# Kernel tuning notes

Measured on AMD Instinct MI355X. Metric: run time of the kernel, lower is better.

The kernel has to match this reference:

```python
import jax, jax.numpy as jnp
import numpy as np

B, NSM, NLG = 64, 400, 196
SM, LG = 512, 1024
D, H, DH = 4, 16, 64
INNER = H * DH
EPS = 1e-5


def setup_inputs() -> dict:
    key = jax.random.key(0)
    ks = iter(jax.random.split(key, 40))
    def rn(shape, s=0.02):
        return jax.random.normal(next(ks), shape, jnp.float32) * s
    inp = {
        "sm_tokens": rn((B, NSM + 1, SM), 1.0),
        "lg_tokens": rn((B, NLG + 1, LG), 1.0),
    }
    def branch(p, din, dout):
        inp[p + "_pin_w"] = rn((D, din, dout))
        inp[p + "_pin_b"] = jnp.zeros((D, dout), jnp.float32)
        inp[p + "_ng"] = jnp.ones((D, dout), jnp.float32)
        inp[p + "_nb"] = jnp.zeros((D, dout), jnp.float32)
        inp[p + "_wq"] = rn((D, dout, INNER))
        inp[p + "_wkv"] = rn((D, dout, 2 * INNER))
        inp[p + "_wo"] = rn((D, INNER, dout))
        inp[p + "_wob"] = jnp.zeros((D, dout), jnp.float32)
        inp[p + "_pout_w"] = rn((D, dout, din))
        inp[p + "_pout_b"] = jnp.zeros((D, din), jnp.float32)
    branch("a", SM, LG)   # sm_attend_lg: project sm->lg, attention in lg_dim
    branch("b", LG, SM)   # lg_attend_sm: project lg->sm, attention in sm_dim
    return inp


def _attn(cls_tok, ctx, ng, nb, wq, wkv, wo, wob):
    # cls_tok: [B,1,dim]; ctx: [B,S,dim]. Matches lucidrains cross_vit Attention:
    # LayerNorm(x) first; kv context = concat(normed_x, context); context NOT normed.
    scale = DH ** -0.5
    mu = cls_tok.mean(-1, keepdims=True)
    var = ((cls_tok - mu) ** 2).mean(-1, keepdims=True)
    xn = (cls_tok - mu) * jax.lax.rsqrt(var + EPS) * ng + nb
    c = jnp.concatenate([xn, ctx], axis=1)             # kv_include_self=True
    q = (xn @ wq).reshape(B, 1, H, DH)
    k, v = jnp.split(c @ wkv, 2, axis=-1)
    k = k.reshape(B, -1, H, DH)
    v = v.reshape(B, -1, H, DH)
    s = jnp.einsum('bqhd,bkhd->bhqk', q, k) * scale     # [B,H,1,S+1]
    p = jax.nn.softmax(s, axis=-1)
    o = jnp.einsum('bhqk,bkhd->bqhd', p, v).reshape(B, 1, INNER)
    return o @ wo + wob


def _forward(sm_tokens, lg_tokens,
             a_pin_w, a_pin_b, a_ng, a_nb, a_wq, a_wkv, a_wo, a_wob, a_pout_w, a_pout_b,
             b_pin_w, b_pin_b, b_ng, b_nb, b_wq, b_wkv, b_wo, b_wob, b_pout_w, b_pout_b):
    sm_cls, sm_patch = sm_tokens[:, :1], sm_tokens[:, 1:]
    lg_cls, lg_patch = lg_tokens[:, :1], lg_tokens[:, 1:]
    for i in range(D):
        x = sm_cls @ a_pin_w[i] + a_pin_b[i]
        x = _attn(x, lg_patch, a_ng[i], a_nb[i], a_wq[i], a_wkv[i], a_wo[i], a_wob[i])
        sm_cls = x @ a_pout_w[i] + a_pout_b[i] + sm_cls
        y = lg_cls @ b_pin_w[i] + b_pin_b[i]
        y = _attn(y, sm_patch, b_ng[i], b_nb[i], b_wq[i], b_wkv[i], b_wo[i], b_wob[i])
        lg_cls = y @ b_pout_w[i] + b_pout_b[i] + lg_cls
    sm_out = jnp.concatenate([sm_cls, sm_patch], axis=1)
    lg_out = jnp.concatenate([lg_cls, lg_patch], axis=1)
    return sm_out, lg_out


def reference(sm_tokens, lg_tokens,
              a_pin_w, a_pin_b, a_ng, a_nb, a_wq, a_wkv, a_wo, a_wob, a_pout_w, a_pout_b,
              b_pin_w, b_pin_b, b_ng, b_nb, b_wq, b_wkv, b_wo, b_wob, b_pout_w, b_pout_b):
    return _forward(sm_tokens, lg_tokens,
                    a_pin_w, a_pin_b, a_ng, a_nb, a_wq, a_wkv, a_wo, a_wob, a_pout_w, a_pout_b,
                    b_pin_w, b_pin_b, b_ng, b_nb, b_wq, b_wkv, b_wo, b_wob, b_pout_w, b_pout_b)
```

## Files before the change

kernel.cpp:

```cpp
#include <hip/hip_runtime.h>
#include <hip/hip_bf16.h>
#include <math.h>

#define B_     64
#define NSM_   400
#define NLG_   196
#define SM_    512
#define LG_    1024
#define H_     16
#define DH_    64
#define INNER_ 1024
#define SSTR   424
#define PSTR   424
#define NJMAX  7

typedef __attribute__((ext_vector_type(8))) short bf16x8;
typedef __attribute__((ext_vector_type(8))) unsigned short u16x8;
typedef __attribute__((ext_vector_type(4))) float f32x4;

__device__ __forceinline__ unsigned short f2b(float f) {
  unsigned u = __float_as_uint(f);
  u = u + 0x7FFFu + ((u >> 16) & 1u);
  return (unsigned short)(u >> 16);
}
__device__ __forceinline__ f32x4 zero4() {
  f32x4 a; a[0] = 0.f; a[1] = 0.f; a[2] = 0.f; a[3] = 0.f; return a;
}
__device__ __forceinline__ bf16x8 ntl8(const unsigned short* p) {
  return __builtin_nontemporal_load((const bf16x8*)p);
}


struct CC2 { const float* tok; float* out; unsigned short* abf; float* cls;
             unsigned short* clsb; int Np1, nf4, shift, tot4; };
struct WTDesc { const float* src; unsigned short* dst; unsigned short* dst2; int K, N; };
struct WTArgs { WTDesc d[10]; int cum[11]; };
__global__ __launch_bounds__(256) void setup1(CC2 ca, CC2 cb, WTArgs W, int nw) {
  __shared__ unsigned short tile[64][68];
  const int tid = threadIdx.x;
  if ((int)blockIdx.x < nw) {
    int bx = blockIdx.x, di = 0;
    while (bx >= W.cum[di + 1]) di++;
    int local = bx - W.cum[di];
    WTDesc g = W.d[di];
    int tn = g.N >> 6;
    int tpl = tn * (g.K >> 6);
    int layer = local / tpl, rem = local % tpl;
    int kt = (rem / tn) * 64, nt = (rem % tn) * 64;
    const float* wp = g.src + (size_t)layer * g.K * g.N;
    unsigned short* op = g.dst + (size_t)layer * g.K * g.N;
    unsigned short* d2 = (g.dst2 && nt < 1024)
                             ? g.dst2 + (size_t)layer * g.K * 1024 : nullptr;
#pragma unroll
    for (int p = 0; p < 4; p++) {
      int r = (tid >> 4) + p * 16;
      int c = (tid & 15) * 4;
      const f32x4 v = __builtin_nontemporal_load(
          (const f32x4*)&wp[(size_t)(kt + r) * g.N + nt + c]);
      ushort4 w4;
      w4.x = f2b(v.x); w4.y = f2b(v.y); w4.z = f2b(v.z); w4.w = f2b(v.w);
      *(ushort4*)&tile[r][c] = w4;
      if (d2) *(ushort4*)&d2[(size_t)(kt + r) * 1024 + nt + c] = w4;
    }
    __syncthreads();
    const int r2 = tid >> 2, cseg = tid & 3;
    u16x8 v0, v1;
#pragma unroll
    for (int i = 0; i < 8; i++) v0[i] = tile[cseg * 16 + i][r2];
#pragma unroll
    for (int i = 0; i < 8; i++) v1[i] = tile[cseg * 16 + 8 + i][r2];
    unsigned short* orow = &op[(size_t)(nt + r2) * g.K + kt + cseg * 16];
    *(u16x8*)&orow[0] = v0;
    *(u16x8*)&orow[8] = v1;
  } else {
    const int nblk = gridDim.x - nw;
    const int total = ca.tot4 + cb.tot4;
    for (int i = ((int)blockIdx.x - nw) * 256 + tid; i < total; i += nblk * 256) {
      CC2 g; int idx;
      if (i < ca.tot4) { g = ca; idx = i; } else { g = cb; idx = i - ca.tot4; }
      int rowg = idx >> g.shift, t = idx & ((1 << g.shift) - 1);
      int bb = rowg / g.Np1, row = rowg - bb * g.Np1;
      const f32x4 v = __builtin_nontemporal_load(&((const f32x4*)g.tok)[idx]);
      __builtin_nontemporal_store(v, &((f32x4*)g.out)[idx]);
      ushort4 w2; w2.x = f2b(v.x); w2.y = f2b(v.y); w2.z = f2b(v.z); w2.w = f2b(v.w);
      if (row > 0) {
        ((ushort4*)g.abf)[(size_t)(bb * (g.Np1 - 1) + row - 1) * g.nf4 + t] = w2;
      } else {
        ((f32x4*)g.cls)[(size_t)bb * g.nf4 + t] = v;
        ((ushort4*)g.clsb)[(size_t)bb * g.nf4 + t] = w2;
      }
    }
  }
}

struct TXArgs { const unsigned short* xbf; unsigned short* xT; int Nctx, dout, xstride, nx, ny, nblk; };
__global__ __launch_bounds__(256) void setup2(TXArgs ta, TXArgs tb) {
  __shared__ unsigned short tile[64][68];
  TXArgs g; int bx = blockIdx.x;
  if (bx < ta.nblk) { g = ta; } else { g = tb; bx -= ta.nblk; }
  int cx = bx % g.nx; int rem = bx / g.nx;
  int jy = rem % g.ny; int b = rem / g.ny;
  int jt = jy * 64, ct = cx * 64;
  const int tid = threadIdx.x;
#pragma unroll
  for (int p = 0; p < 4; p++) {
    int row = (tid >> 4) + p * 16;
    int c = (tid & 15) * 4;
    int j = jt + row;
    ushort4 v;
    if (j < g.Nctx) v = *(const ushort4*)&g.xbf[((size_t)b * g.Nctx + j) * g.dout + ct + c];
    else { v.x = 0; v.y = 0; v.z = 0; v.w = 0; }
    *(ushort4*)&tile[row][c] = v;
  }
  __syncthreads();
  const int r2 = tid >> 2, jseg = tid & 3;
  if (jt + jseg * 16 < g.xstride) {
    u16x8 v0, v1;
#pragma unroll
    for (int i = 0; i < 8; i++) v0[i] = tile[jseg * 16 + i][r2];
#pragma unroll
    for (int i = 0; i < 8; i++) v1[i] = tile[jseg * 16 + 8 + i][r2];
    unsigned short* orow = &g.xT[((size_t)b * g.dout + ct + r2) * g.xstride + jt + jseg * 16];
    *(u16x8*)&orow[0] = v0;
    *(u16x8*)&orow[8] = v1;
  }
}

struct SGDesc {
  const unsigned short* A; const unsigned short* WT; const float* bias;
  float* Cf; unsigned short* Cbf; const float* Rf;
  int K, N;
  float* outF; int ostride;
};
struct SGArgs { SGDesc d[4]; int cum[5]; int nd; };
__global__ __launch_bounds__(256) void sg_wide(SGArgs W) {
  int bx = blockIdx.x, di = 0;
  while (di < W.nd - 1 && bx >= W.cum[di + 1]) di++;
  SGDesc g = W.d[di];
  const int n0 = (bx - W.cum[di]) * 16;
  const int tid = threadIdx.x;
  const int lane = tid & 63, mt = tid >> 6;
  const int r16 = lane & 15, kv8 = (lane >> 4) * 8;
  f32x4 acc0 = zero4(), acc1 = zero4();
  const unsigned short* wp = &g.WT[(size_t)(n0 + r16) * g.K + kv8];
  const unsigned short* ap = &g.A[(size_t)(mt * 16 + r16) * g.K + kv8];
  const int K = g.K;
#pragma unroll 2
  for (int k0 = 0; k0 < K; k0 += 64) {
    acc0 = __builtin_amdgcn_mfma_f32_16x16x32_bf16(*(const bf16x8*)&ap[k0],
                                                   ntl8(&wp[k0]), acc0, 0, 0, 0);
    acc1 = __builtin_amdgcn_mfma_f32_16x16x32_bf16(*(const bf16x8*)&ap[k0 + 32],
                                                   ntl8(&wp[k0 + 32]), acc1, 0, 0, 0);
  }
  const int rbase = (lane >> 4) * 4;
#pragma unroll
  for (int rr = 0; rr < 4; rr++) {
    int r = mt * 16 + rbase + rr, c = n0 + r16;
    float v = acc0[rr] + acc1[rr];
    if (g.bias) v += g.bias[c];
    if (g.Rf) v += g.Rf[(size_t)r * g.N + c];
    if (g.Cf)  g.Cf[(size_t)r * g.N + c] = v;
    if (g.Cbf) g.Cbf[(size_t)r * g.N + c] = f2b(v);
    if (g.outF) g.outF[(size_t)r * g.ostride + c] = v;
  }
}

struct LNArgs { const float* x; unsigned short* xnb; const float* ng; const float* nb; int dim; };
__global__ __launch_bounds__(256) void ln2(LNArgs la, LNArgs lb) {
  LNArgs g = ((int)blockIdx.x < 64) ? la : lb;
  int b = blockIdx.x & 63, t = threadIdx.x;
  __shared__ float rs[4], rq[4], bc[2];
  const float* xp = g.x + (size_t)b * g.dim;
  float s = 0.f, sq = 0.f;
  for (int c = t; c < g.dim; c += 256) {
    float v = xp[c];
    s += v; sq += v * v;
  }
#pragma unroll
  for (int off = 32; off >= 1; off >>= 1) {
    s += __shfl_down(s, off);
    sq += __shfl_down(sq, off);
  }
  int w = t >> 6;
  if ((t & 63) == 0) { rs[w] = s; rq[w] = sq; }
  __syncthreads();
  if (t == 0) {
    float ts = rs[0] + rs[1] + rs[2] + rs[3];
    float tq = rq[0] + rq[1] + rq[2] + rq[3];
    float mu = ts / g.dim;
    float var = tq / g.dim - mu * mu;
    bc[0] = mu; bc[1] = rsqrtf(var + 1e-5f);
  }
  __syncthreads();
  float mu = bc[0], r = bc[1];
  for (int c = t; c < g.dim; c += 256)
    g.xnb[(size_t)b * g.dim + c] = f2b((xp[c] - mu) * r * g.ng[c] + g.nb[c]);
}

struct QTArgs { const unsigned short* qb16; const unsigned short* wkvnb;
                unsigned short* qt; int dout, ntiles, nblk; };
__global__ __launch_bounds__(256) void qtilde3(QTArgs ga, QTArgs gb) {
  QTArgs g; int bx = blockIdx.x;
  if (bx < ga.nblk) g = ga; else { g = gb; bx -= ga.nblk; }
  const int h = bx / g.ntiles, nt = bx - h * g.ntiles;
  const int n0 = nt * 16;
  const int tid = threadIdx.x, lane = tid & 63, mt = tid >> 6;
  const int r16 = lane & 15, kv8 = (lane >> 4) * 8;
  const unsigned short* ap = g.qb16 + (size_t)(mt * 16 + r16) * INNER_ + h * 64 + kv8;
  const unsigned short* bp = g.wkvnb + (size_t)(n0 + r16) * 1024 + h * 64 + kv8;
  f32x4 acc0 = zero4(), acc1 = zero4();
  acc0 = __builtin_amdgcn_mfma_f32_16x16x32_bf16(*(const bf16x8*)&ap[0],
                                                 *(const bf16x8*)&bp[0], acc0, 0, 0, 0);
  acc1 = __builtin_amdgcn_mfma_f32_16x16x32_bf16(*(const bf16x8*)&ap[32],
                                                 *(const bf16x8*)&bp[32], acc1, 0, 0, 0);
  const int rbase = (lane >> 4) * 4;
#pragma unroll
  for (int rr = 0; rr < 4; rr++) {
    int b = mt * 16 + rbase + rr;
    g.qt[((size_t)b * 16 + h) * g.dout + n0 + r16] = f2b(acc0[rr] + acc1[rr]);
  }
}

struct SArgs { const unsigned short* qt; const unsigned short* xbf; float* S;
               int dout, Nctx, ntj, nbj, nblk; };
__global__ __launch_bounds__(256) void s_gemm(SArgs ga, SArgs gb) {
  SArgs g; int bx;
  if ((int)blockIdx.x < ga.nblk) { g = ga; bx = blockIdx.x; }
  else { g = gb; bx = blockIdx.x - ga.nblk; }
  const int b = bx / g.nbj, jq = bx - b * g.nbj;
  const int tid = threadIdx.x, lane = tid & 63, w = tid >> 6;
  const int jt = jq * 4 + w;
  if (jt >= g.ntj) return;
  const int r16 = lane & 15, kv8 = (lane >> 4) * 8;
  const unsigned short* ap = g.qt + ((size_t)b * 16 + r16) * g.dout + kv8;
  const unsigned short* bp = g.xbf + ((size_t)b * g.Nctx + jt * 16 + r16) * g.dout + kv8;
  f32x4 acc0 = zero4(), acc1 = zero4();
  const int K = g.dout;
#pragma unroll 2
  for (int k0 = 0; k0 < K; k0 += 64) {
    acc0 = __builtin_amdgcn_mfma_f32_16x16x32_bf16(*(const bf16x8*)&ap[k0],
                                                   *(const bf16x8*)&bp[k0], acc0, 0, 0, 0);
    acc1 = __builtin_amdgcn_mfma_f32_16x16x32_bf16(*(const bf16x8*)&ap[k0 + 32],
                                                   *(const bf16x8*)&bp[k0 + 32], acc1, 0, 0, 0);
  }
  const int rbase = (lane >> 4) * 4;
#pragma unroll
  for (int rr = 0; rr < 4; rr++)
    g.S[((size_t)b * 16 + rbase + rr) * SSTR + jt * 16 + r16] = acc0[rr] + acc1[rr];
}

struct UArgs {
  const float* S; const float* qb; const float* kvc; const unsigned short* xT;
  unsigned short* u; float* pcls; int dout, Nctx, Npad, xstride, ntc, nblk;
};
__global__ __launch_bounds__(256) void usoftmax(UArgs ga, UArgs gb) {
  __shared__ unsigned short p_s[16 * PSTR];
  UArgs g; int bx;
  if ((int)blockIdx.x < ga.nblk) { g = ga; bx = blockIdx.x; }
  else { g = gb; bx = blockIdx.x - ga.nblk; }
  const int b = bx / g.ntc, ct = bx - b * g.ntc;
  const int t = threadIdx.x, lane = t & 63, w = t >> 6;
  for (int hh = 0; hh < 4; hh++) {
    const int h = w * 4 + hh;
    const float* Sp = g.S + ((size_t)b * 16 + h) * SSTR;
    float sc = g.qb[(size_t)b * 1024 + h * 64 + lane] * g.kvc[(size_t)b * 2048 + h * 64 + lane];
#pragma unroll
    for (int o = 32; o >= 1; o >>= 1) sc += __shfl_down(sc, o);
    sc = __shfl(sc, 0) * 0.125f;
    float sv[NJMAX];
    float mr = -1e30f;
#pragma unroll
    for (int ji = 0; ji < NJMAX; ji++) {
      int j = ji * 64 + lane;
      sv[ji] = (j < g.Nctx) ? Sp[j] * 0.125f : -1e30f;
      mr = fmaxf(mr, sv[ji]);
    }
#pragma unroll
    for (int o = 32; o >= 1; o >>= 1) mr = fmaxf(mr, __shfl_down(mr, o));
    mr = __shfl(mr, 0);
    const float m = fmaxf(mr, sc);
    float es = 0.f;
#pragma unroll
    for (int ji = 0; ji < NJMAX; ji++) {
      int j = ji * 64 + lane;
      float e = (j < g.Nctx) ? expf(sv[ji] - m) : 0.f;
      sv[ji] = e; es += e;
    }
#pragma unroll
    for (int o = 32; o >= 1; o >>= 1) es += __shfl_down(es, o);
    es = __shfl(es, 0);
    const float ecls = expf(sc - m);
    const float inv = 1.f / (es + ecls);
#pragma unroll
    for (int ji = 0; ji < NJMAX; ji++) {
      int j = ji * 64 + lane;
      if (j < g.Npad) p_s[h * PSTR + j] = (j < g.Nctx) ? f2b(sv[ji] * inv) : (unsigned short)0;
    }
    if (ct == 0 && lane == 0) g.pcls[b * 16 + h] = ecls * inv;
  }
  __syncthreads();
  const int r16 = lane & 15, kv8 = (lane >> 4) * 8, rbase = (lane >> 4) * 4;
  const int c0 = ct * 64 + w * 16;
  f32x4 acc0 = zero4(), acc1 = zero4();
  const unsigned short* bp = g.xT + ((size_t)b * g.dout + c0 + r16) * g.xstride + kv8;
  const unsigned short* apl = &p_s[r16 * PSTR + kv8];
  const int Kp = g.Npad;
  int k0 = 0;
  for (; k0 + 64 <= Kp; k0 += 64) {
    acc0 = __builtin_amdgcn_mfma_f32_16x16x32_bf16(*(const bf16x8*)&apl[k0],
                                                   *(const bf16x8*)&bp[k0], acc0, 0, 0, 0);
    acc1 = __builtin_amdgcn_mfma_f32_16x16x32_bf16(*(const bf16x8*)&apl[k0 + 32],
                                                   *(const bf16x8*)&bp[k0 + 32], acc1, 0, 0, 0);
  }
  if (k0 < Kp)
    acc0 = __builtin_amdgcn_mfma_f32_16x16x32_bf16(*(const bf16x8*)&apl[k0],
                                                   *(const bf16x8*)&bp[k0], acc0, 0, 0, 0);
#pragma unroll
  for (int rr = 0; rr < 4; rr++)
    g.u[((size_t)b * 16 + rbase + rr) * g.dout + c0 + r16] = f2b(acc0[rr] + acc1[rr]);
}

struct OArgs {
  const unsigned short* u; const unsigned short* WTkv; const float* kvc; const float* pcls;
  unsigned short* ob; int dout;
};
__global__ __launch_bounds__(256) void ogemm_w(OArgs ga, OArgs gb) {
  OArgs g; int bx = blockIdx.x;
  if (bx < 64) { g = ga; } else { g = gb; bx -= 64; }
  const int h = bx >> 2, dt = bx & 3;
  const int tid = threadIdx.x, lane = tid & 63, mt = tid >> 6;
  const int r16 = lane & 15, kv8 = (lane >> 4) * 8;
  const int dout = g.dout;
  f32x4 acc0 = zero4(), acc1 = zero4();
  const unsigned short* wp = &g.WTkv[(size_t)(1024 + h * 64 + dt * 16 + r16) * dout + kv8];
  const unsigned short* up = &g.u[((size_t)(mt * 16 + r16) * 16 + h) * dout + kv8];
#pragma unroll 2
  for (int k0 = 0; k0 < dout; k0 += 64) {
    acc0 = __builtin_amdgcn_mfma_f32_16x16x32_bf16(*(const bf16x8*)&up[k0],
                                                   ntl8(&wp[k0]), acc0, 0, 0, 0);
    acc1 = __builtin_amdgcn_mfma_f32_16x16x32_bf16(*(const bf16x8*)&up[k0 + 32],
                                                   ntl8(&wp[k0 + 32]), acc1, 0, 0, 0);
  }
  const int rbase = (lane >> 4) * 4;
#pragma unroll
  for (int rr = 0; rr < 4; rr++) {
    int bi = mt * 16 + rbase + rr;
    int d = h * 64 + dt * 16 + r16;
    float v = acc0[rr] + acc1[rr] + g.pcls[bi * 16 + h] * g.kvc[(size_t)bi * 2048 + 1024 + d];
    g.ob[(size_t)bi * INNER_ + d] = f2b(v);
  }
}

extern "C" void kernel_launch(void* const* d_in, const int* in_sizes, int n_in,
                              void* d_out, int out_size, void* d_ws, size_t ws_size,
                              hipStream_t stream) {
  const float* sm_tokens = (const float*)d_in[0];
  const float* lg_tokens = (const float*)d_in[1];
  const float* a_pin_w  = (const float*)d_in[2];  const float* a_pin_b  = (const float*)d_in[3];
  const float* a_ng     = (const float*)d_in[4];  const float* a_nb     = (const float*)d_in[5];
  const float* a_wq     = (const float*)d_in[6];  const float* a_wkv    = (const float*)d_in[7];
  const float* a_wo     = (const float*)d_in[8];  const float* a_wob    = (const float*)d_in[9];
  const float* a_pout_w = (const float*)d_in[10]; const float* a_pout_b = (const float*)d_in[11];
  const float* b_pin_w  = (const float*)d_in[12]; const float* b_pin_b  = (const float*)d_in[13];
  const float* b_ng     = (const float*)d_in[14]; const float* b_nb     = (const float*)d_in[15];
  const float* b_wq     = (const float*)d_in[16]; const float* b_wkv    = (const float*)d_in[17];
  const float* b_wo     = (const float*)d_in[18]; const float* b_wob    = (const float*)d_in[19];
  const float* b_pout_w = (const float*)d_in[20]; const float* b_pout_b = (const float*)d_in[21];

  float* out = (float*)d_out;
  char* ws = (char*)d_ws;
  size_t off = 0;
  auto alloc = [&](size_t bytes) -> void* {
    void* pt = ws + off;
    off += (bytes + 255) & ~(size_t)255;
    return pt;
  };
  unsigned short* Abf_lg = (unsigned short*)alloc(((size_t)B_ * NLG_ + 32) * LG_ * 2);
  unsigned short* Abf_sm = (unsigned short*)alloc(((size_t)B_ * NSM_ + 32) * SM_ * 2);
  unsigned short* xT_lg  = (unsigned short*)alloc((size_t)B_ * LG_ * 224 * 2);
  unsigned short* xT_sm  = (unsigned short*)alloc((size_t)B_ * SM_ * 416 * 2);
  unsigned short* WTkv_a = (unsigned short*)alloc((size_t)4 * 2048 * LG_ * 2);
  unsigned short* WTkv_b = (unsigned short*)alloc((size_t)4 * 2048 * SM_ * 2);
  unsigned short* wkvnb_a = (unsigned short*)alloc((size_t)4 * LG_ * 1024 * 2);
  unsigned short* wkvnb_b = (unsigned short*)alloc((size_t)4 * SM_ * 1024 * 2);
  unsigned short* WTpin_a = (unsigned short*)alloc((size_t)4 * SM_ * LG_ * 2);
  unsigned short* WTpin_b = (unsigned short*)alloc((size_t)4 * LG_ * SM_ * 2);
  unsigned short* WTwq_a  = (unsigned short*)alloc((size_t)4 * LG_ * INNER_ * 2);
  unsigned short* WTwq_b  = (unsigned short*)alloc((size_t)4 * SM_ * INNER_ * 2);
  unsigned short* WTwo_a  = (unsigned short*)alloc((size_t)4 * INNER_ * LG_ * 2);
  unsigned short* WTwo_b  = (unsigned short*)alloc((size_t)4 * INNER_ * SM_ * 2);
  unsigned short* WTpout_a = (unsigned short*)alloc((size_t)4 * LG_ * SM_ * 2);
  unsigned short* WTpout_b = (unsigned short*)alloc((size_t)4 * SM_ * LG_ * 2);
  unsigned short* qt_a = (unsigned short*)alloc((size_t)B_ * 16 * LG_ * 2);
  unsigned short* qt_b = (unsigned short*)alloc((size_t)B_ * 16 * SM_ * 2);
  float* S_a = (float*)alloc((size_t)B_ * 16 * SSTR * 4);
  float* S_b = (float*)alloc((size_t)B_ * 16 * SSTR * 4);
  unsigned short* u_a  = (unsigned short*)alloc((size_t)B_ * 16 * LG_ * 2);
  unsigned short* u_b  = (unsigned short*)alloc((size_t)B_ * 16 * SM_ * 2);
  float* pcls_a = (float*)alloc((size_t)B_ * 16 * 4);
  float* pcls_b = (float*)alloc((size_t)B_ * 16 * 4);
  float* cls_sm = (float*)alloc((size_t)B_ * SM_ * 4);
  float* cls_lg = (float*)alloc((size_t)B_ * LG_ * 4);
  unsigned short* clsb_sm = (unsigned short*)alloc((size_t)B_ * SM_ * 2);
  unsigned short* clsb_lg = (unsigned short*)alloc((size_t)B_ * LG_ * 2);
  float* xbuf_a = (float*)alloc((size_t)B_ * LG_ * 4);
  float* xbuf_b = (float*)alloc((size_t)B_ * SM_ * 4);
  unsigned short* xnb_a = (unsigned short*)alloc((size_t)B_ * LG_ * 2);
  unsigned short* xnb_b = (unsigned short*)alloc((size_t)B_ * SM_ * 2);
  float* qbuf_a = (float*)alloc((size_t)B_ * INNER_ * 4);
  float* qbuf_b = (float*)alloc((size_t)B_ * INNER_ * 4);
  unsigned short* qb16_a = (unsigned short*)alloc((size_t)B_ * INNER_ * 2);
  unsigned short* qb16_b = (unsigned short*)alloc((size_t)B_ * INNER_ * 2);
  float* kvc_a  = (float*)alloc((size_t)B_ * 2048 * 4);
  float* kvc_b  = (float*)alloc((size_t)B_ * 2048 * 4);
  unsigned short* obufb_a = (unsigned short*)alloc((size_t)B_ * INNER_ * 2);
  unsigned short* obufb_b = (unsigned short*)alloc((size_t)B_ * INNER_ * 2);
  unsigned short* t1b_a = (unsigned short*)alloc((size_t)B_ * LG_ * 2);
  unsigned short* t1b_b = (unsigned short*)alloc((size_t)B_ * SM_ * 2);
  (void)ws_size; (void)in_sizes; (void)n_in; (void)out_size;

  const size_t sm_elems = (size_t)B_ * (NSM_ + 1) * SM_;

  CC2 ca{sm_tokens, out, Abf_sm, cls_sm, clsb_sm, NSM_ + 1, SM_ / 4, 7,
         (int)(sm_elems / 4)};
  CC2 cb{lg_tokens, out + sm_elems, Abf_lg, cls_lg, clsb_lg, NLG_ + 1, LG_ / 4, 8,
         (int)((size_t)B_ * (NLG_ + 1) * LG_ / 4)};
  WTArgs W;
  W.d[0] = {a_wkv,    WTkv_a,   wkvnb_a, LG_, 2048};
  W.d[1] = {b_wkv,    WTkv_b,   wkvnb_b, SM_, 2048};
  W.d[2] = {a_pin_w,  WTpin_a,  nullptr, SM_, LG_};
  W.d[3] = {b_pin_w,  WTpin_b,  nullptr, LG_, SM_};
  W.d[4] = {a_wq,     WTwq_a,   nullptr, LG_, INNER_};
  W.d[5] = {b_wq,     WTwq_b,   nullptr, SM_, INNER_};
  W.d[6] = {a_wo,     WTwo_a,   nullptr, INNER_, LG_};
  W.d[7] = {b_wo,     WTwo_b,   nullptr, INNER_, SM_};
  W.d[8] = {a_pout_w, WTpout_a, nullptr, LG_, SM_};
  W.d[9] = {b_pout_w, WTpout_b, nullptr, SM_, LG_};
  W.cum[0] = 0;
  for (int i = 0; i < 10; i++)
    W.cum[i + 1] = W.cum[i] + (W.d[i].K / 64) * (W.d[i].N / 64) * 4;
  setup1<<<W.cum[10] + 2048, 256, 0, stream>>>(ca, cb, W, W.cum[10]);
  TXArgs txa{Abf_lg, xT_lg, NLG_, LG_, 224, LG_ / 64, 4, B_ * (LG_ / 64) * 4};
  TXArgs txb{Abf_sm, xT_sm, NSM_, SM_, 416, SM_ / 64, 7, B_ * (SM_ / 64) * 7};
  setup2<<<txa.nblk + txb.nblk, 256, 0, stream>>>(txa, txb);

  for (int l = 0; l < 4; l++) {
    const unsigned short* WTpin_al = WTpin_a + (size_t)l * SM_ * LG_;
    const unsigned short* WTpin_bl = WTpin_b + (size_t)l * LG_ * SM_;
    const unsigned short* WTwq_al  = WTwq_a  + (size_t)l * LG_ * INNER_;
    const unsigned short* WTwq_bl  = WTwq_b  + (size_t)l * SM_ * INNER_;
    const unsigned short* WTkv_al  = WTkv_a  + (size_t)l * 2048 * LG_;
    const unsigned short* WTkv_bl  = WTkv_b  + (size_t)l * 2048 * SM_;
    const unsigned short* wkvnb_al = wkvnb_a + (size_t)l * LG_ * 1024;
    const unsigned short* wkvnb_bl = wkvnb_b + (size_t)l * SM_ * 1024;
    const unsigned short* WTwo_al  = WTwo_a  + (size_t)l * INNER_ * LG_;
    const unsigned short* WTwo_bl  = WTwo_b  + (size_t)l * INNER_ * SM_;
    const unsigned short* WTpout_al = WTpout_a + (size_t)l * LG_ * SM_;
    const unsigned short* WTpout_bl = WTpout_b + (size_t)l * SM_ * LG_;

    SGArgs Gp; Gp.nd = 2;
    Gp.d[0] = {clsb_sm, WTpin_al, a_pin_b + (size_t)l * LG_, xbuf_a, nullptr, nullptr, SM_, LG_, nullptr, 0};
    Gp.d[1] = {clsb_lg, WTpin_bl, b_pin_b + (size_t)l * SM_, xbuf_b, nullptr, nullptr, LG_, SM_, nullptr, 0};
    Gp.cum[0] = 0; Gp.cum[1] = LG_ / 16; Gp.cum[2] = LG_ / 16 + SM_ / 16;
    sg_wide<<<Gp.cum[2], 256, 0, stream>>>(Gp);
    LNArgs la{xbuf_a, xnb_a, a_ng + (size_t)l * LG_, a_nb + (size_t)l * LG_, LG_};
    LNArgs lb{xbuf_b, xnb_b, b_ng + (size_t)l * SM_, b_nb + (size_t)l * SM_, SM_};
    ln2<<<128, 256, 0, stream>>>(la, lb);
    SGArgs Gq; Gq.nd = 4;
    Gq.d[0] = {xnb_a, WTwq_al, nullptr, qbuf_a, qb16_a, nullptr, LG_, INNER_, nullptr, 0};
    Gq.d[1] = {xnb_a, WTkv_al, nullptr, kvc_a,  nullptr, nullptr, LG_, 2048, nullptr, 0};
    Gq.d[2] = {xnb_b, WTwq_bl, nullptr, qbuf_b, qb16_b, nullptr, SM_, INNER_, nullptr, 0};
    Gq.d[3] = {xnb_b, WTkv_bl, nullptr, kvc_b,  nullptr, nullptr, SM_, 2048, nullptr, 0};
    Gq.cum[0] = 0; Gq.cum[1] = 64; Gq.cum[2] = 192; Gq.cum[3] = 256; Gq.cum[4] = 384;
    sg_wide<<<384, 256, 0, stream>>>(Gq);
    QTArgs qa{qb16_a, wkvnb_al, qt_a, LG_, LG_ / 16, 16 * (LG_ / 16)};
    QTArgs qb{qb16_b, wkvnb_bl, qt_b, SM_, SM_ / 16, 16 * (SM_ / 16)};
    qtilde3<<<qa.nblk + qb.nblk, 256, 0, stream>>>(qa, qb);
    SArgs sa{qt_a, Abf_lg, S_a, LG_, NLG_, 14, 4, B_ * 4};
    SArgs sb{qt_b, Abf_sm, S_b, SM_, NSM_, 26, 7, B_ * 7};
    s_gemm<<<sa.nblk + sb.nblk, 256, 0, stream>>>(sa, sb);
    UArgs ua{S_a, qbuf_a, kvc_a, xT_lg, u_a, pcls_a, LG_, NLG_, 224, 224, LG_ / 64, B_ * (LG_ / 64)};
    UArgs ub{S_b, qbuf_b, kvc_b, xT_sm, u_b, pcls_b, SM_, NSM_, 416, 416, SM_ / 64, B_ * (SM_ / 64)};
    usoftmax<<<ua.nblk + ub.nblk, 256, 0, stream>>>(ua, ub);
    OArgs oa{u_a, WTkv_al, kvc_a, pcls_a, obufb_a, LG_};
    OArgs ob{u_b, WTkv_bl, kvc_b, pcls_b, obufb_b, SM_};
    ogemm_w<<<128, 256, 0, stream>>>(oa, ob);
    SGArgs Gw; Gw.nd = 2;
    Gw.d[0] = {obufb_a, WTwo_al, a_wob + (size_t)l * LG_, nullptr, t1b_a, nullptr, INNER_, LG_, nullptr, 0};
    Gw.d[1] = {obufb_b, WTwo_bl, b_wob + (size_t)l * SM_, nullptr, t1b_b, nullptr, INNER_, SM_, nullptr, 0};
    Gw.cum[0] = 0; Gw.cum[1] = LG_ / 16; Gw.cum[2] = LG_ / 16 + SM_ / 16;
    sg_wide<<<Gw.cum[2], 256, 0, stream>>>(Gw);
    float* outF_a = (l == 3) ? out : nullptr;
    float* outF_b = (l == 3) ? out + sm_elems : nullptr;
    SGArgs Gr; Gr.nd = 2;
    Gr.d[0] = {t1b_a, WTpout_al, a_pout_b + (size_t)l * SM_, cls_sm, clsb_sm, cls_sm, LG_, SM_,
               outF_a, (NSM_ + 1) * SM_};
    Gr.d[1] = {t1b_b, WTpout_bl, b_pout_b + (size_t)l * LG_, cls_lg, clsb_lg, cls_lg, SM_, LG_,
               outF_b, (NLG_ + 1) * LG_};
    Gr.cum[0] = 0; Gr.cum[1] = SM_ / 16; Gr.cum[2] = SM_ / 16 + LG_ / 16;
    sg_wide<<<Gr.cum[2], 256, 0, stream>>>(Gr);
  }
}
```

Measured before the change: 531.5 us.

## Split fused softmax+PV kernel into separate softmax and GEMM kernels

Before, each PV-GEMM block recomputed the full softmax for all 16 heads of its batch. That softmax work was repeated across every column tile (16 or 8 times per batch). Now a standalone softmax kernel runs once per (head, batch), writes bf16 probabilities to a global buffer, and a separate GEMM kernel reads them. The weight loads in the GEMMs also switch from nontemporal loads to plain loads. This adds one extra launch and a global round-trip for P in exchange for removing the redundant softmax work.

```diff
diff --git a/kernel.cpp b/kernel.cpp
--- a/kernel.cpp
+++ b/kernel.cpp
@@ -12,7 +12,6 @@
 #define INNER_ 1024
 #define SSTR   424
 #define PSTR   424
-#define NJMAX  7
 
 typedef __attribute__((ext_vector_type(8))) short bf16x8;
 typedef __attribute__((ext_vector_type(8))) unsigned short u16x8;
@@ -25,9 +24,6 @@
 }
 __device__ __forceinline__ f32x4 zero4() {
   f32x4 a; a[0] = 0.f; a[1] = 0.f; a[2] = 0.f; a[3] = 0.f; return a;
-}
-__device__ __forceinline__ bf16x8 ntl8(const unsigned short* p) {
-  return __builtin_nontemporal_load((const bf16x8*)p);
 }
 
 
@@ -148,9 +144,9 @@
 #pragma unroll 2
   for (int k0 = 0; k0 < K; k0 += 64) {
     acc0 = __builtin_amdgcn_mfma_f32_16x16x32_bf16(*(const bf16x8*)&ap[k0],
-                                                   ntl8(&wp[k0]), acc0, 0, 0, 0);
+                                                   *(const bf16x8*)&wp[k0], acc0, 0, 0, 0);
     acc1 = __builtin_amdgcn_mfma_f32_16x16x32_bf16(*(const bf16x8*)&ap[k0 + 32],
-                                                   ntl8(&wp[k0 + 32]), acc1, 0, 0, 0);
+                                                   *(const bf16x8*)&wp[k0 + 32], acc1, 0, 0, 0);
   }
   const int rbase = (lane >> 4) * 4;
 #pragma unroll
@@ -249,71 +245,76 @@
     g.S[((size_t)b * 16 + rbase + rr) * SSTR + jt * 16 + r16] = acc0[rr] + acc1[rr];
 }
 
-struct UArgs {
-  const float* S; const float* qb; const float* kvc; const unsigned short* xT;
-  unsigned short* u; float* pcls; int dout, Nctx, Npad, xstride, ntc, nblk;
-};
-__global__ __launch_bounds__(256) void usoftmax(UArgs ga, UArgs gb) {
-  __shared__ unsigned short p_s[16 * PSTR];
-  UArgs g; int bx;
-  if ((int)blockIdx.x < ga.nblk) { g = ga; bx = blockIdx.x; }
-  else { g = gb; bx = blockIdx.x - ga.nblk; }
-  const int b = bx / g.ntc, ct = bx - b * g.ntc;
-  const int t = threadIdx.x, lane = t & 63, w = t >> 6;
-  for (int hh = 0; hh < 4; hh++) {
-    const int h = w * 4 + hh;
-    const float* Sp = g.S + ((size_t)b * 16 + h) * SSTR;
-    float sc = g.qb[(size_t)b * 1024 + h * 64 + lane] * g.kvc[(size_t)b * 2048 + h * 64 + lane];
-#pragma unroll
-    for (int o = 32; o >= 1; o >>= 1) sc += __shfl_down(sc, o);
-    sc = __shfl(sc, 0) * 0.125f;
-    float sv[NJMAX];
-    float mr = -1e30f;
-#pragma unroll
-    for (int ji = 0; ji < NJMAX; ji++) {
-      int j = ji * 64 + lane;
-      sv[ji] = (j < g.Nctx) ? Sp[j] * 0.125f : -1e30f;
-      mr = fmaxf(mr, sv[ji]);
-    }
-#pragma unroll
-    for (int o = 32; o >= 1; o >>= 1) mr = fmaxf(mr, __shfl_down(mr, o));
-    mr = __shfl(mr, 0);
-    const float m = fmaxf(mr, sc);
-    float es = 0.f;
-#pragma unroll
-    for (int ji = 0; ji < NJMAX; ji++) {
-      int j = ji * 64 + lane;
-      float e = (j < g.Nctx) ? expf(sv[ji] - m) : 0.f;
-      sv[ji] = e; es += e;
-    }
-#pragma unroll
-    for (int o = 32; o >= 1; o >>= 1) es += __shfl_down(es, o);
-    es = __shfl(es, 0);
-    const float ecls = expf(sc - m);
-    const float inv = 1.f / (es + ecls);
-#pragma unroll
-    for (int ji = 0; ji < NJMAX; ji++) {
-      int j = ji * 64 + lane;
-      if (j < g.Npad) p_s[h * PSTR + j] = (j < g.Nctx) ? f2b(sv[ji] * inv) : (unsigned short)0;
-    }
-    if (ct == 0 && lane == 0) g.pcls[b * 16 + h] = ecls * inv;
-  }
-  __syncthreads();
+struct SMArgs { const float* S; const float* qb; const float* kvc;
+                unsigned short* p; float* pcls; int Nctx, Npad; };
+__global__ __launch_bounds__(256) void softmax_p2(SMArgs ga, SMArgs gb) {
+  SMArgs g = blockIdx.z ? gb : ga;
+  const int h = blockIdx.x, b = blockIdx.y;
+  const int t = threadIdx.x;
+  __shared__ float red[4], bc;
+  float sc = 0.f;
+  if (t < 64) sc = g.qb[(size_t)b * INNER_ + h * 64 + t] * g.kvc[(size_t)b * 2048 + h * 64 + t];
+#pragma unroll
+  for (int o = 32; o >= 1; o >>= 1) sc += __shfl_down(sc, o);
+  if (t == 0) bc = sc * 0.125f;
+  __syncthreads();
+  const float scls = bc;
+  const float* Sp = g.S + ((size_t)b * 16 + h) * SSTR;
+
+  float sraw[2] = {-1e30f, -1e30f};
+#pragma unroll
+  for (int u2 = 0; u2 < 2; u2++) {
+    int j = t + u2 * 256;
+    if (j < g.Nctx) sraw[u2] = Sp[j] * 0.125f;
+  }
+  float mx = fmaxf(fmaxf(sraw[0], sraw[1]), scls);
+#pragma unroll
+  for (int o = 32; o >= 1; o >>= 1) mx = fmaxf(mx, __shfl_down(mx, o));
+  if ((t & 63) == 0) red[t >> 6] = mx;
+  __syncthreads();
+  mx = fmaxf(fmaxf(red[0], red[1]), fmaxf(red[2], red[3]));
+  __syncthreads();
+
+  float e0 = (t < g.Nctx) ? expf(sraw[0] - mx) : 0.f;
+  float e1 = (t + 256 < g.Nctx) ? expf(sraw[1] - mx) : 0.f;
+  float ecls = expf(scls - mx);
+  float ls = e0 + e1;
+#pragma unroll
+  for (int o = 32; o >= 1; o >>= 1) ls += __shfl_down(ls, o);
+  if ((t & 63) == 0) red[t >> 6] = ls;
+  __syncthreads();
+  const float denom = red[0] + red[1] + red[2] + red[3] + ecls;
+  const float inv = 1.f / denom;
+
+  unsigned short* pp = g.p + ((size_t)b * 16 + h) * PSTR;
+  if (t < g.Nctx) pp[t] = f2b(e0 * inv);
+  if (t + 256 < g.Nctx) pp[t + 256] = f2b(e1 * inv);
+  for (int j = g.Nctx + t; j < g.Npad; j += 256) pp[j] = 0;
+  if (t == 0) g.pcls[b * 16 + h] = ecls * inv;
+}
+
+struct UG { const unsigned short* p; const unsigned short* xT; unsigned short* u;
+            int dout, Npad, xstride, ntx; };
+__global__ __launch_bounds__(256) void ugemm2(UG ga, UG gb) {
+  UG g; int bx = blockIdx.x;
+  if (bx < ga.ntx) g = ga; else { g = gb; bx -= ga.ntx; }
+  const int b = blockIdx.y;
+  const int tid = threadIdx.x, lane = tid & 63, w = tid >> 6;
+  const int c0 = bx * 64 + w * 16;
   const int r16 = lane & 15, kv8 = (lane >> 4) * 8, rbase = (lane >> 4) * 4;
-  const int c0 = ct * 64 + w * 16;
+  const unsigned short* ap = g.p + ((size_t)b * 16 + r16) * PSTR + kv8;
+  const unsigned short* bp = g.xT + ((size_t)b * g.dout + c0 + r16) * g.xstride + kv8;
   f32x4 acc0 = zero4(), acc1 = zero4();
-  const unsigned short* bp = g.xT + ((size_t)b * g.dout + c0 + r16) * g.xstride + kv8;
-  const unsigned short* apl = &p_s[r16 * PSTR + kv8];
   const int Kp = g.Npad;
   int k0 = 0;
   for (; k0 + 64 <= Kp; k0 += 64) {
-    acc0 = __builtin_amdgcn_mfma_f32_16x16x32_bf16(*(const bf16x8*)&apl[k0],
+    acc0 = __builtin_amdgcn_mfma_f32_16x16x32_bf16(*(const bf16x8*)&ap[k0],
                                                    *(const bf16x8*)&bp[k0], acc0, 0, 0, 0);
-    acc1 = __builtin_amdgcn_mfma_f32_16x16x32_bf16(*(const bf16x8*)&apl[k0 + 32],
+    acc1 = __builtin_amdgcn_mfma_f32_16x16x32_bf16(*(const bf16x8*)&ap[k0 + 32],
                                                    *(const bf16x8*)&bp[k0 + 32], acc1, 0, 0, 0);
   }
   if (k0 < Kp)
-    acc0 = __builtin_amdgcn_mfma_f32_16x16x32_bf16(*(const bf16x8*)&apl[k0],
+    acc0 = __builtin_amdgcn_mfma_f32_16x16x32_bf16(*(const bf16x8*)&ap[k0],
                                                    *(const bf16x8*)&bp[k0], acc0, 0, 0, 0);
 #pragma unroll
   for (int rr = 0; rr < 4; rr++)
@@ -337,9 +338,9 @@
 #pragma unroll 2
   for (int k0 = 0; k0 < dout; k0 += 64) {
     acc0 = __builtin_amdgcn_mfma_f32_16x16x32_bf16(*(const bf16x8*)&up[k0],
-                                                   ntl8(&wp[k0]), acc0, 0, 0, 0);
+                                                   *(const bf16x8*)&wp[k0], acc0, 0, 0, 0);
     acc1 = __builtin_amdgcn_mfma_f32_16x16x32_bf16(*(const bf16x8*)&up[k0 + 32],
-                                                   ntl8(&wp[k0 + 32]), acc1, 0, 0, 0);
+                                                   *(const bf16x8*)&wp[k0 + 32], acc1, 0, 0, 0);
   }
   const int rbase = (lane >> 4) * 4;
 #pragma unroll
@@ -395,6 +396,8 @@
   unsigned short* qt_b = (unsigned short*)alloc((size_t)B_ * 16 * SM_ * 2);
   float* S_a = (float*)alloc((size_t)B_ * 16 * SSTR * 4);
   float* S_b = (float*)alloc((size_t)B_ * 16 * SSTR * 4);
+  unsigned short* p_a = (unsigned short*)alloc((size_t)B_ * 16 * PSTR * 2);
+  unsigned short* p_b = (unsigned short*)alloc((size_t)B_ * 16 * PSTR * 2);
   unsigned short* u_a  = (unsigned short*)alloc((size_t)B_ * 16 * LG_ * 2);
   unsigned short* u_b  = (unsigned short*)alloc((size_t)B_ * 16 * SM_ * 2);
   float* pcls_a = (float*)alloc((size_t)B_ * 16 * 4);
@@ -479,9 +482,12 @@
     SArgs sa{qt_a, Abf_lg, S_a, LG_, NLG_, 14, 4, B_ * 4};
     SArgs sb{qt_b, Abf_sm, S_b, SM_, NSM_, 26, 7, B_ * 7};
     s_gemm<<<sa.nblk + sb.nblk, 256, 0, stream>>>(sa, sb);
-    UArgs ua{S_a, qbuf_a, kvc_a, xT_lg, u_a, pcls_a, LG_, NLG_, 224, 224, LG_ / 64, B_ * (LG_ / 64)};
-    UArgs ub{S_b, qbuf_b, kvc_b, xT_sm, u_b, pcls_b, SM_, NSM_, 416, 416, SM_ / 64, B_ * (SM_ / 64)};
-    usoftmax<<<ua.nblk + ub.nblk, 256, 0, stream>>>(ua, ub);
+    SMArgs ma{S_a, qbuf_a, kvc_a, p_a, pcls_a, NLG_, 224};
+    SMArgs mb{S_b, qbuf_b, kvc_b, p_b, pcls_b, NSM_, 416};
+    softmax_p2<<<dim3(H_, B_, 2), 256, 0, stream>>>(ma, mb);
+    UG ua{p_a, xT_lg, u_a, LG_, 224, 224, LG_ / 64};
+    UG ub{p_b, xT_sm, u_b, SM_, 416, 416, SM_ / 64};
+    ugemm2<<<dim3(LG_ / 64 + SM_ / 64, B_), 256, 0, stream>>>(ua, ub);
     OArgs oa{u_a, WTkv_al, kvc_a, pcls_a, obufb_a, LG_};
     OArgs ob{u_b, WTkv_bl, kvc_b, pcls_b, obufb_b, SM_};
     ogemm_w<<<128, 256, 0, stream>>>(oa, ob);
```

Measured after the change: 496.0 us, median of 3. 6.7% less time.
